# Kernel optimization log

Measured on AMD Instinct MI355X. Metric: run time of the kernel, lower is better.

Reference implementation:

```python
import jax, jax.numpy as jnp
import numpy as np

N_PARTITIONS = 16
EPS = 1e-5


def setup_inputs() -> dict:
    key = jax.random.key(0)
    ks = jax.random.split(key, 8)
    B, in_size = 4096, 4096
    d = in_size // N_PARTITIONS  # 256
    s = 1.0 / np.sqrt(d)
    return {
        "x": jax.random.normal(ks[0], (B, in_size), dtype=jnp.float32),
        "WQ_w": jax.random.normal(ks[1], (d, d), dtype=jnp.float32) * s,
        "WQ_b": jax.random.normal(ks[2], (d,), dtype=jnp.float32) * s,
        "WK_w": jax.random.normal(ks[3], (d, d), dtype=jnp.float32) * s,
        "WK_b": jax.random.normal(ks[4], (d,), dtype=jnp.float32) * s,
        "WV_w": jax.random.normal(ks[5], (d, d), dtype=jnp.float32) * s,
        "WV_b": jax.random.normal(ks[6], (d,), dtype=jnp.float32) * s,
        "bn_gamma": jnp.ones((in_size,), dtype=jnp.float32),
        "bn_beta": jnp.zeros((in_size,), dtype=jnp.float32),
    }


def reference(x, WQ_w, WQ_b, WK_w, WK_b, WV_w, WV_b, bn_gamma, bn_beta):
    B, in_size = x.shape
    p = N_PARTITIONS
    d = in_size // p
    scale = jnp.asarray(np.sqrt(d), dtype=x.dtype)

    # BatchNorm1d in training mode: batch statistics, biased variance
    mean = jnp.mean(x, axis=0)
    var = jnp.mean((x - mean) ** 2, axis=0)
    x_norm = (x - mean) * jax.lax.rsqrt(var + EPS) * bn_gamma + bn_beta

    # Split features into partitions: [B, p, d]; shared Linear per partition.
    xp = x_norm.reshape(B, p, d)
    # Torch loop builds Q[b, :, i] = WQ(x_part_i)[b]  ->  [B, d, p]
    Q = jnp.einsum('bpd,ed->bep', xp, WQ_w) + WQ_b[None, :, None]
    K = jnp.einsum('bpd,ed->bep', xp, WK_w) + WK_b[None, :, None]
    V = jnp.einsum('bpd,ed->bep', xp, WV_w) + WV_b[None, :, None]

    # bmm(Q, K^T): [B, d, d], softmax over last axis, bmm with V: [B, d, p]
    dot = jnp.einsum('bep,bfp->bef', Q, K) / scale
    attn = jax.nn.softmax(dot, axis=2)
    prod = jnp.einsum('bef,bfp->bep', attn, V)

    # torch.cat(prod[:, i] for i in range(d), dim=1) == row-major flatten of [B, d, p]
    out = prod.reshape(B, d * p) + x
    return out
```

## Files before the change

### kernel.cpp

```cpp
#include <hip/hip_runtime.h>
#include <hip/hip_bf16.h>
#include <stdint.h>

typedef __attribute__((ext_vector_type(8))) short short8;
typedef __attribute__((ext_vector_type(4))) short short4_t;
typedef __attribute__((ext_vector_type(4))) float f32x4;
typedef __attribute__((ext_vector_type(2))) unsigned int u32x2;
typedef __attribute__((ext_vector_type(4))) unsigned int u32x4;

union FragU { u32x4 u; short8 s; };
union Frag2U { u32x2 u; short4_t s; };

__device__ __forceinline__ unsigned short f2bf(float f) {
  union { float f; uint32_t u; } v; v.f = f;
  uint32_t u = v.u;
  return (unsigned short)((u + 0x7FFFu + ((u >> 16) & 1u)) >> 16);
}

__device__ __forceinline__ unsigned pk2(float a, float b) {
  return (unsigned)f2bf(a) | ((unsigned)f2bf(b) << 16);
}

__device__ __forceinline__ void gload_lds16(const void* g, void* l) {
  __builtin_amdgcn_global_load_lds(
      (const __attribute__((address_space(1))) unsigned int*)g,
      (__attribute__((address_space(3))) unsigned int*)l, 16, 0, 0);
}

#if defined(__has_builtin)
#if __has_builtin(__builtin_amdgcn_mfma_f32_16x16x16bf16_1k)
#define HAVE_MFMA16_BUILTIN 1
#endif
#endif

__device__ __forceinline__ f32x4 mfma16(u32x2 a, u32x2 b, f32x4 c) {
#ifdef HAVE_MFMA16_BUILTIN
  Frag2U ua, ub;
  ua.u = a; ub.u = b;
  return __builtin_amdgcn_mfma_f32_16x16x16bf16_1k(ua.s, ub.s, c, 0, 0, 0);
#else
  asm volatile("s_nop 1\n\t"
               "v_mfma_f32_16x16x16_bf16 %0, %1, %2, %0\n\t"
               "s_nop 7\n\t"
               "s_nop 7"
               : "+v"(c) : "v"(a), "v"(b));
  return c;
#endif
}

__global__ __launch_bounds__(256) void k_stats(const float* __restrict__ x,
                                               float* __restrict__ psum,
                                               float* __restrict__ psq) {
  int t = threadIdx.x;
  int cb = blockIdx.x & 3;
  int ck = blockIdx.x >> 2;
  int c0 = cb * 1024 + t * 4;
  f32x4 s = {0.f, 0.f, 0.f, 0.f}, q = {0.f, 0.f, 0.f, 0.f};
  const float* base = x + (size_t)ck * 64 * 4096 + c0;
#pragma unroll 4
  for (int r = 0; r < 64; ++r) {
    f32x4 v = *(const f32x4*)(base + (size_t)r * 4096);
    s += v;
    q += v * v;
  }
  *(f32x4*)(psum + (size_t)ck * 4096 + c0) = s;
  *(f32x4*)(psq + (size_t)ck * 4096 + c0) = q;
}

__global__ __launch_bounds__(256) void k_finalize(const float* __restrict__ psum,
                                                  const float* __restrict__ psq,
                                                  const float* __restrict__ gamma,
                                                  const float* __restrict__ beta,
                                                  float* __restrict__ An,
                                                  float* __restrict__ Bn) {
  int c = blockIdx.x * 256 + threadIdx.x;
  float s = 0.f, q = 0.f;
  for (int k = 0; k < 64; ++k) {
    s += psum[k * 4096 + c];
    q += psq[k * 4096 + c];
  }
  float mean = s * (1.0f / 4096.0f);
  float var = q * (1.0f / 4096.0f) - mean * mean;
  float a = gamma[c] * rsqrtf(var + 1e-5f);
  An[c] = a;
  Bn[c] = beta[c] - mean * a;
}

__global__ __launch_bounds__(256) void k_qkv(
    const float* __restrict__ x, const float* __restrict__ An, const float* __restrict__ Bn,
    const float* __restrict__ WQ, const float* __restrict__ bQ,
    const float* __restrict__ WK, const float* __restrict__ bK,
    const float* __restrict__ WV, const float* __restrict__ bV,
    unsigned short* __restrict__ Qt, unsigned short* __restrict__ Kt,
    unsigned short* __restrict__ Vo) {
  __shared__ unsigned short Asm[128 * 256];
  __shared__ unsigned short Bsm[128 * 256];
  int t = threadIdx.x;
  int mb = blockIdx.x >> 1, nb = blockIdx.x & 1;

  for (int i = 0; i < 16; ++i) {
    int m = i * 8 + (t >> 5);
    int k0 = (t & 31) * 8;
    size_t r = (size_t)(mb * 128 + m);
    const float* xs = x + r * 256 + k0;
    f32x4 v0 = *(const f32x4*)(xs), v1 = *(const f32x4*)(xs + 4);
    int c = ((int)(r & 15)) * 256 + k0;
    f32x4 a0 = *(const f32x4*)(An + c), a1 = *(const f32x4*)(An + c + 4);
    f32x4 b0 = *(const f32x4*)(Bn + c), b1 = *(const f32x4*)(Bn + c + 4);
    f32x4 n0 = v0 * a0 + b0, n1 = v1 * a1 + b1;
    union { u32x4 u; unsigned short h[8]; } pk;
    pk.h[0] = f2bf(n0.x); pk.h[1] = f2bf(n0.y); pk.h[2] = f2bf(n0.z); pk.h[3] = f2bf(n0.w);
    pk.h[4] = f2bf(n1.x); pk.h[5] = f2bf(n1.y); pk.h[6] = f2bf(n1.z); pk.h[7] = f2bf(n1.w);
    int off = m * 512 + ((k0 * 2) ^ ((m & 7) << 4));
    *(u32x4*)((char*)Asm + off) = pk.u;
  }

  int w = t >> 6, ln = t & 63, lr = ln & 15, g = ln >> 4;
  int wm = (w >> 1) * 64, wn = (w & 1) * 64;

#pragma unroll
  for (int mat = 0; mat < 3; ++mat) {
    const float* W = (mat == 0) ? WQ : ((mat == 1) ? WK : WV);
    const float* bias = (mat == 0) ? bQ : ((mat == 1) ? bK : bV);
    unsigned short* Out = (mat == 0) ? Qt : ((mat == 1) ? Kt : Vo);
    float scale = (mat == 0) ? 0.0625f : 1.0f;

    __syncthreads();
    for (int i = 0; i < 16; ++i) {
      int n = i * 8 + (t >> 5);
      int k0 = (t & 31) * 8;
      const float* wsrc = W + (size_t)(nb * 128 + n) * 256 + k0;
      f32x4 v0 = *(const f32x4*)(wsrc), v1 = *(const f32x4*)(wsrc + 4);
      union { u32x4 u; unsigned short h[8]; } pk;
      pk.h[0] = f2bf(v0.x); pk.h[1] = f2bf(v0.y); pk.h[2] = f2bf(v0.z); pk.h[3] = f2bf(v0.w);
      pk.h[4] = f2bf(v1.x); pk.h[5] = f2bf(v1.y); pk.h[6] = f2bf(v1.z); pk.h[7] = f2bf(v1.w);
      int off = n * 512 + ((k0 * 2) ^ ((n & 7) << 4));
      *(u32x4*)((char*)Bsm + off) = pk.u;
    }
    __syncthreads();

    f32x4 acc[4][4];
    f32x4 z4 = {0.f, 0.f, 0.f, 0.f};
#pragma unroll
    for (int a_ = 0; a_ < 4; ++a_)
#pragma unroll
      for (int b_ = 0; b_ < 4; ++b_) acc[a_][b_] = z4;

    for (int kk = 0; kk < 8; ++kk) {
      FragU af[4], bfr[4];
#pragma unroll
      for (int mt = 0; mt < 4; ++mt) {
        int m = wm + mt * 16 + lr;
        af[mt].u = *(const u32x4*)((const char*)Asm + m * 512 + ((kk * 64 + g * 16) ^ ((m & 7) << 4)));
      }
#pragma unroll
      for (int nt = 0; nt < 4; ++nt) {
        int n = wn + nt * 16 + lr;
        bfr[nt].u = *(const u32x4*)((const char*)Bsm + n * 512 + ((kk * 64 + g * 16) ^ ((n & 7) << 4)));
      }
#pragma unroll
      for (int mt = 0; mt < 4; ++mt)
#pragma unroll
        for (int nt = 0; nt < 4; ++nt)
          acc[mt][nt] = __builtin_amdgcn_mfma_f32_16x16x32_bf16(af[mt].s, bfr[nt].s, acc[mt][nt], 0, 0, 0);
    }

#pragma unroll
    for (int nt = 0; nt < 4; ++nt) {
      int ccol = nb * 128 + wn + nt * 16 + lr;
      float bv = bias[ccol];
#pragma unroll
      for (int mt = 0; mt < 4; ++mt) {
        int rbase = mb * 128 + wm + mt * 16;
        int b_ = rbase >> 4;
#pragma unroll
        for (int rg = 0; rg < 4; ++rg) {
          int p_ = g * 4 + rg;
          unsigned short val = f2bf((acc[mt][nt][rg] + bv) * scale);
          if (mat < 2) {
            Out[(size_t)b_ * 4096 + (size_t)ccol * 16 + p_] = val;
          } else {
            Out[(size_t)(rbase + p_) * 256 + ccol] = val;
          }
        }
      }
    }
  }
}

#define LQT 0
#define LKT 8192
#define LVS 16384
#define LTOT 24576

__global__ __launch_bounds__(256, 3) void k_attn(
    const unsigned short* __restrict__ Qtg, const unsigned short* __restrict__ Ktg,
    const unsigned short* __restrict__ Vg, const float* __restrict__ x,
    float* __restrict__ out) {
  __shared__ char lds[LTOT];
  int b = blockIdx.x;
  int t = threadIdx.x;
  int w = t >> 6, ln = t & 63, lr = ln & 15, g = ln >> 4;

  for (int i = w; i < 24; i += 4) {
    const unsigned short* srcmat;
    unsigned srcbyte;
    int region;
    if (i < 8) {
      srcmat = Qtg;
      srcbyte = (unsigned)b * 8192 + i * 1024 + ln * 16;
      region = LQT + i * 1024;
    } else if (i < 16) {
      int ii = i - 8;
      srcmat = Ktg;
      srcbyte = (unsigned)b * 8192 + ii * 1024 + ln * 16;
      region = LKT + ii * 1024;
    } else {
      int ii = i - 16;
      srcmat = Vg;
      int d = ii * 1024 + ln * 16;
      int p = d >> 9;
      int cc = d & 511;
      srcbyte = (unsigned)b * 8192 + p * 512 + (unsigned)(cc ^ ((p & 7) << 4));
      region = LVS + ii * 1024;
    }
    gload_lds16((const char*)srcmat + srcbyte, &lds[region]);
  }
  __syncthreads();

  u32x2 qf[4];
#pragma unroll
  for (int nt = 0; nt < 4; ++nt)
    qf[nt] = *(const u32x2*)(&lds[LQT + (w * 64 + nt * 16 + lr) * 32 + g * 8]);

  u32x2 ones;
  ones.x = 0x3F803F80u; ones.y = 0x3F803F80u;

  f32x4 accT[4], dden[4];
  f32x4 z4 = {0.f, 0.f, 0.f, 0.f};
#pragma unroll
  for (int nt = 0; nt < 4; ++nt) { accT[nt] = z4; dden[nt] = z4; }

  for (int c = 0; c < 8; ++c) {
#pragma unroll
    for (int mt_ = 0; mt_ < 2; ++mt_) {
      u32x2 kf = *(const u32x2*)(&lds[LKT + (c * 32 + mt_ * 16 + lr) * 32 + g * 8]);

      f32x4 st[4];
#pragma unroll
      for (int nt = 0; nt < 4; ++nt)
        st[nt] = mfma16(kf, qf[nt], z4);

      u32x2 vf = *(const u32x2*)(
          &lds[LVS + lr * 512 + ((c * 64 + mt_ * 32 + g * 8) ^ ((lr & 7) << 4))]);

#pragma unroll
      for (int nt = 0; nt < 4; ++nt) {
        float e0 = __expf(st[nt].x);
        float e1 = __expf(st[nt].y);
        float e2 = __expf(st[nt].z);
        float e3 = __expf(st[nt].w);
        u32x2 pB;
        pB.x = pk2(e0, e1);
        pB.y = pk2(e2, e3);
        accT[nt] = mfma16(vf, pB, accT[nt]);
        dden[nt] = mfma16(ones, pB, dden[nt]);
      }
    }
  }

  size_t rowbase = (size_t)b * 4096;
#pragma unroll
  for (int nt = 0; nt < 4; ++nt) {
    int e = w * 64 + nt * 16 + lr;
    size_t col = (size_t)e * 16 + g * 4;
    float inv = 1.0f / dden[nt].x;
    f32x4 xr = *(const f32x4*)(x + rowbase + col);
    f32x4 o = accT[nt] * inv + xr;
    *(f32x4*)(out + rowbase + col) = o;
  }
}

extern "C" void kernel_launch(void* const* d_in, const int* in_sizes, int n_in,
                              void* d_out, int out_size, void* d_ws, size_t ws_size,
                              hipStream_t stream) {
  const float* x = (const float*)d_in[0];
  const float* WQ = (const float*)d_in[1];
  const float* bQ = (const float*)d_in[2];
  const float* WK = (const float*)d_in[3];
  const float* bK = (const float*)d_in[4];
  const float* WV = (const float*)d_in[5];
  const float* bV = (const float*)d_in[6];
  const float* gamma = (const float*)d_in[7];
  const float* beta = (const float*)d_in[8];
  float* out = (float*)d_out;
  char* ws = (char*)d_ws;

  float* psum = (float*)(ws);
  float* psq = (float*)(ws + (1 << 20));
  float* An = (float*)(ws + (2 << 20));
  float* Bn = (float*)(ws + (2 << 20) + (16 << 10));
  unsigned short* Qt = (unsigned short*)(ws + (size_t)(4 << 20));
  unsigned short* Kt = (unsigned short*)(ws + (size_t)(4 << 20) + (32u << 20));
  unsigned short* Vo = (unsigned short*)(ws + (size_t)(4 << 20) + (64u << 20));

  hipLaunchKernelGGL(k_stats, dim3(256), dim3(256), 0, stream, x, psum, psq);
  hipLaunchKernelGGL(k_finalize, dim3(16), dim3(256), 0, stream, psum, psq, gamma, beta, An, Bn);
  hipLaunchKernelGGL(k_qkv, dim3(1024), dim3(256), 0, stream, x, An, Bn,
                     WQ, bQ, WK, bK, WV, bV, Qt, Kt, Vo);
  hipLaunchKernelGGL(k_attn, dim3(4096), dim3(256), 0, stream, Qt, Kt, Vo, x, out);
}
```

Measured before the change: 152.7 us.

## Pre-convert weights to bf16, read B fragments from global, use scalar softmax denominator

A new kernel converts the three weight matrices to bf16 once per call. The QKV kernel now uses 64-row tiles across all 256 output columns and reads weight fragments straight from global/L2 instead of staging them in LDS. This halves LDS use and removes the per-block weight conversion and its barriers. In the attention kernel, the MFMA against a ones vector used for the softmax denominator is replaced by per-lane fp32 sums plus cross-lane shuffles, which drops one MFMA per tile but adds VALU adds.

```diff
diff --git a/kernel.cpp b/kernel.cpp
--- a/kernel.cpp
+++ b/kernel.cpp
@@ -46,6 +46,21 @@
                : "+v"(c) : "v"(a), "v"(b));
   return c;
 #endif
+}
+
+__global__ __launch_bounds__(256) void k_wconv(const float* __restrict__ WQ,
+                                               const float* __restrict__ WK,
+                                               const float* __restrict__ WV,
+                                               unsigned short* __restrict__ Wbf) {
+  int mat = blockIdx.x >> 5;
+  int i = blockIdx.x & 31;
+  const float* W = (mat == 0) ? WQ : ((mat == 1) ? WK : WV);
+  int off = i * 2048 + threadIdx.x * 8;
+  f32x4 v0 = *(const f32x4*)(W + off), v1 = *(const f32x4*)(W + off + 4);
+  u32x4 pk;
+  pk.x = pk2(v0.x, v0.y); pk.y = pk2(v0.z, v0.w);
+  pk.z = pk2(v1.x, v1.y); pk.w = pk2(v1.z, v1.w);
+  *(u32x4*)(Wbf + (size_t)mat * 65536 + off) = pk;
 }
 
 __global__ __launch_bounds__(256) void k_stats(const float* __restrict__ x,
@@ -88,56 +103,40 @@
 
 __global__ __launch_bounds__(256) void k_qkv(
     const float* __restrict__ x, const float* __restrict__ An, const float* __restrict__ Bn,
-    const float* __restrict__ WQ, const float* __restrict__ bQ,
-    const float* __restrict__ WK, const float* __restrict__ bK,
-    const float* __restrict__ WV, const float* __restrict__ bV,
+    const unsigned short* __restrict__ Wbf,
+    const float* __restrict__ bQ, const float* __restrict__ bK, const float* __restrict__ bV,
     unsigned short* __restrict__ Qt, unsigned short* __restrict__ Kt,
     unsigned short* __restrict__ Vo) {
-  __shared__ unsigned short Asm[128 * 256];
-  __shared__ unsigned short Bsm[128 * 256];
+  __shared__ unsigned short Asm[64 * 256];
   int t = threadIdx.x;
-  int mb = blockIdx.x >> 1, nb = blockIdx.x & 1;
-
-  for (int i = 0; i < 16; ++i) {
+  int mb = blockIdx.x;
+
+  for (int i = 0; i < 8; ++i) {
     int m = i * 8 + (t >> 5);
     int k0 = (t & 31) * 8;
-    size_t r = (size_t)(mb * 128 + m);
+    size_t r = (size_t)(mb * 64 + m);
     const float* xs = x + r * 256 + k0;
     f32x4 v0 = *(const f32x4*)(xs), v1 = *(const f32x4*)(xs + 4);
     int c = ((int)(r & 15)) * 256 + k0;
     f32x4 a0 = *(const f32x4*)(An + c), a1 = *(const f32x4*)(An + c + 4);
     f32x4 b0 = *(const f32x4*)(Bn + c), b1 = *(const f32x4*)(Bn + c + 4);
     f32x4 n0 = v0 * a0 + b0, n1 = v1 * a1 + b1;
-    union { u32x4 u; unsigned short h[8]; } pk;
-    pk.h[0] = f2bf(n0.x); pk.h[1] = f2bf(n0.y); pk.h[2] = f2bf(n0.z); pk.h[3] = f2bf(n0.w);
-    pk.h[4] = f2bf(n1.x); pk.h[5] = f2bf(n1.y); pk.h[6] = f2bf(n1.z); pk.h[7] = f2bf(n1.w);
+    u32x4 pk;
+    pk.x = pk2(n0.x, n0.y); pk.y = pk2(n0.z, n0.w);
+    pk.z = pk2(n1.x, n1.y); pk.w = pk2(n1.z, n1.w);
     int off = m * 512 + ((k0 * 2) ^ ((m & 7) << 4));
-    *(u32x4*)((char*)Asm + off) = pk.u;
-  }
+    *(u32x4*)((char*)Asm + off) = pk;
+  }
+  __syncthreads();
 
   int w = t >> 6, ln = t & 63, lr = ln & 15, g = ln >> 4;
-  int wm = (w >> 1) * 64, wn = (w & 1) * 64;
+  int wn = w * 64;
 
 #pragma unroll
   for (int mat = 0; mat < 3; ++mat) {
-    const float* W = (mat == 0) ? WQ : ((mat == 1) ? WK : WV);
+    const unsigned short* W = Wbf + (size_t)mat * 65536;
     const float* bias = (mat == 0) ? bQ : ((mat == 1) ? bK : bV);
-    unsigned short* Out = (mat == 0) ? Qt : ((mat == 1) ? Kt : Vo);
     float scale = (mat == 0) ? 0.0625f : 1.0f;
-
-    __syncthreads();
-    for (int i = 0; i < 16; ++i) {
-      int n = i * 8 + (t >> 5);
-      int k0 = (t & 31) * 8;
-      const float* wsrc = W + (size_t)(nb * 128 + n) * 256 + k0;
-      f32x4 v0 = *(const f32x4*)(wsrc), v1 = *(const f32x4*)(wsrc + 4);
-      union { u32x4 u; unsigned short h[8]; } pk;
-      pk.h[0] = f2bf(v0.x); pk.h[1] = f2bf(v0.y); pk.h[2] = f2bf(v0.z); pk.h[3] = f2bf(v0.w);
-      pk.h[4] = f2bf(v1.x); pk.h[5] = f2bf(v1.y); pk.h[6] = f2bf(v1.z); pk.h[7] = f2bf(v1.w);
-      int off = n * 512 + ((k0 * 2) ^ ((n & 7) << 4));
-      *(u32x4*)((char*)Bsm + off) = pk.u;
-    }
-    __syncthreads();
 
     f32x4 acc[4][4];
     f32x4 z4 = {0.f, 0.f, 0.f, 0.f};
@@ -146,17 +145,18 @@
 #pragma unroll
       for (int b_ = 0; b_ < 4; ++b_) acc[a_][b_] = z4;
 
+#pragma unroll
     for (int kk = 0; kk < 8; ++kk) {
       FragU af[4], bfr[4];
 #pragma unroll
-      for (int mt = 0; mt < 4; ++mt) {
-        int m = wm + mt * 16 + lr;
-        af[mt].u = *(const u32x4*)((const char*)Asm + m * 512 + ((kk * 64 + g * 16) ^ ((m & 7) << 4)));
-      }
-#pragma unroll
       for (int nt = 0; nt < 4; ++nt) {
         int n = wn + nt * 16 + lr;
-        bfr[nt].u = *(const u32x4*)((const char*)Bsm + n * 512 + ((kk * 64 + g * 16) ^ ((n & 7) << 4)));
+        bfr[nt].u = *(const u32x4*)((const char*)W + (size_t)n * 512 + kk * 64 + g * 16);
+      }
+#pragma unroll
+      for (int mt = 0; mt < 4; ++mt) {
+        int m = mt * 16 + lr;
+        af[mt].u = *(const u32x4*)((const char*)Asm + m * 512 + ((kk * 64 + g * 16) ^ ((m & 7) << 4)));
       }
 #pragma unroll
       for (int mt = 0; mt < 4; ++mt)
@@ -167,20 +167,20 @@
 
 #pragma unroll
     for (int nt = 0; nt < 4; ++nt) {
-      int ccol = nb * 128 + wn + nt * 16 + lr;
-      float bv = bias[ccol];
+      int ccol = wn + nt * 16 + lr;
+      float bvs = bias[ccol] * scale;
 #pragma unroll
       for (int mt = 0; mt < 4; ++mt) {
-        int rbase = mb * 128 + wm + mt * 16;
+        int rbase = mb * 64 + mt * 16;
         int b_ = rbase >> 4;
 #pragma unroll
         for (int rg = 0; rg < 4; ++rg) {
           int p_ = g * 4 + rg;
-          unsigned short val = f2bf((acc[mt][nt][rg] + bv) * scale);
+          unsigned short val = f2bf(acc[mt][nt][rg] * scale + bvs);
           if (mat < 2) {
-            Out[(size_t)b_ * 4096 + (size_t)ccol * 16 + p_] = val;
+            (mat == 0 ? Qt : Kt)[(size_t)b_ * 4096 + (size_t)ccol * 16 + p_] = val;
           } else {
-            Out[(size_t)(rbase + p_) * 256 + ccol] = val;
+            Vo[(size_t)(rbase + p_) * 256 + ccol] = val;
           }
         }
       }
@@ -233,13 +233,11 @@
   for (int nt = 0; nt < 4; ++nt)
     qf[nt] = *(const u32x2*)(&lds[LQT + (w * 64 + nt * 16 + lr) * 32 + g * 8]);
 
-  u32x2 ones;
-  ones.x = 0x3F803F80u; ones.y = 0x3F803F80u;
-
-  f32x4 accT[4], dden[4];
+  f32x4 accT[4];
+  float denp[4];
   f32x4 z4 = {0.f, 0.f, 0.f, 0.f};
 #pragma unroll
-  for (int nt = 0; nt < 4; ++nt) { accT[nt] = z4; dden[nt] = z4; }
+  for (int nt = 0; nt < 4; ++nt) { accT[nt] = z4; denp[nt] = 0.f; }
 
   for (int c = 0; c < 8; ++c) {
 #pragma unroll
@@ -260,13 +258,21 @@
         float e1 = __expf(st[nt].y);
         float e2 = __expf(st[nt].z);
         float e3 = __expf(st[nt].w);
+        denp[nt] += (e0 + e1) + (e2 + e3);
         u32x2 pB;
         pB.x = pk2(e0, e1);
         pB.y = pk2(e2, e3);
         accT[nt] = mfma16(vf, pB, accT[nt]);
-        dden[nt] = mfma16(ones, pB, dden[nt]);
       }
     }
+  }
+
+#pragma unroll
+  for (int nt = 0; nt < 4; ++nt) {
+    float v = denp[nt];
+    v += __shfl_xor(v, 16);
+    v += __shfl_xor(v, 32);
+    denp[nt] = v;
   }
 
   size_t rowbase = (size_t)b * 4096;
@@ -274,7 +280,7 @@
   for (int nt = 0; nt < 4; ++nt) {
     int e = w * 64 + nt * 16 + lr;
     size_t col = (size_t)e * 16 + g * 4;
-    float inv = 1.0f / dden[nt].x;
+    float inv = 1.0f / denp[nt];
     f32x4 xr = *(const f32x4*)(x + rowbase + col);
     f32x4 o = accT[nt] * inv + xr;
     *(f32x4*)(out + rowbase + col) = o;
@@ -300,13 +306,15 @@
   float* psq = (float*)(ws + (1 << 20));
   float* An = (float*)(ws + (2 << 20));
   float* Bn = (float*)(ws + (2 << 20) + (16 << 10));
+  unsigned short* Wbf = (unsigned short*)(ws + (3 << 20));
   unsigned short* Qt = (unsigned short*)(ws + (size_t)(4 << 20));
   unsigned short* Kt = (unsigned short*)(ws + (size_t)(4 << 20) + (32u << 20));
   unsigned short* Vo = (unsigned short*)(ws + (size_t)(4 << 20) + (64u << 20));
 
+  hipLaunchKernelGGL(k_wconv, dim3(96), dim3(256), 0, stream, WQ, WK, WV, Wbf);
   hipLaunchKernelGGL(k_stats, dim3(256), dim3(256), 0, stream, x, psum, psq);
   hipLaunchKernelGGL(k_finalize, dim3(16), dim3(256), 0, stream, psum, psq, gamma, beta, An, Bn);
   hipLaunchKernelGGL(k_qkv, dim3(1024), dim3(256), 0, stream, x, An, Bn,
-                     WQ, bQ, WK, bK, WV, bV, Qt, Kt, Vo);
+                     Wbf, bQ, bK, bV, Qt, Kt, Vo);
   hipLaunchKernelGGL(k_attn, dim3(4096), dim3(256), 0, stream, Qt, Kt, Vo, x, out);
 }
```

Result: no change. 153.2 us (+0.4%).
